# Performance work log

Hardware: AMD Instinct MI355X
Metric: run time of the kernel (lower is better)

The kernel has to match this reference:

```python
import jax, jax.numpy as jnp
import numpy as np


def _conv(x, kernel):
    # x: [N, C, H, W], kernel: [O, I, kh, kw]; torch conv2d padding=1 (symmetric both dims)
    return jax.lax.conv_general_dilated(
        x, kernel, window_strides=(1, 1), padding=((1, 1), (1, 1)),
        dimension_numbers=("NCHW", "OIHW", "NCHW"))


def setup_inputs() -> dict:
    key = jax.random.key(0)
    k1, k2 = jax.random.split(key)
    shape = (2, 7, 7, 3, 256, 256)  # bs, ah, aw, c, h, w
    infer = jax.random.normal(k1, shape, dtype=jnp.float32)
    ref = jax.random.normal(k2, shape, dtype=jnp.float32)
    return {"infer": infer, "ref": ref}


def reference(infer, ref):
    bs, ah, aw, c, h, w = infer.shape
    x = infer.reshape(bs * ah * aw, c, h, w)
    y = ref.reshape(bs * ah * aw, c, h, w)
    # fixed gradient kernels, identical across all 3x3 in/out channel pairs
    kh = jnp.broadcast_to(
        jnp.array([-0.5, 0.0, 0.5], jnp.float32).reshape(1, 1, 1, 3), (3, 3, 1, 3))
    kv = jnp.broadcast_to(
        jnp.array([-0.5, 0.0, 0.5], jnp.float32).reshape(1, 1, 3, 1), (3, 3, 3, 1))
    # torch padding=1 on a (1,3) kernel -> output (h+2, w); on (3,1) -> (h, w+2)
    loss_h = jnp.mean(jnp.abs(_conv(x, kh) - _conv(y, kh)))
    loss_v = jnp.mean(jnp.abs(_conv(x, kv) - _conv(y, kv)))
    return (loss_h + loss_v) / 2.0
```

## Files before the change

kernel.cpp:

```cpp
#include <hip/hip_runtime.h>


#define TH 32
#define NSTRIP 8
#define NIMG 98
#define W 256
#define IMG_CH_STRIDE 65536

__global__ __launch_bounds__(256) void detail_loss_kernel(
    const float* __restrict__ x, const float* __restrict__ y,
    float* __restrict__ out) {
  __shared__ float Dsh[TH + 2][W];

  const int n     = blockIdx.x / NSTRIP;
  const int strip = blockIdx.x % NSTRIP;
  const int h0    = strip * TH;
  const int tid   = threadIdx.x;
  const int sub   = tid >> 6;
  const int w4    = (tid & 63) << 2;

  const size_t img_off = (size_t)n * 3 * IMG_CH_STRIDE;
  const float* xb = x + img_off;
  const float* yb = y + img_off;

  for (int base = 0; base < TH + 2; base += 4) {
    int lr = base + sub;
    if (lr < TH + 2) {
      int row = h0 - 1 + lr;
      float4 d = make_float4(0.f, 0.f, 0.f, 0.f);
      if (row >= 0 && row < 256) {
        int off = row * W + w4;
        #pragma unroll
        for (int c = 0; c < 3; ++c) {
          float4 xv = *(const float4*)(xb + (size_t)c * IMG_CH_STRIDE + off);
          float4 yv = *(const float4*)(yb + (size_t)c * IMG_CH_STRIDE + off);
          d.x += xv.x - yv.x;
          d.y += xv.y - yv.y;
          d.z += xv.z - yv.z;
          d.w += xv.w - yv.w;
        }
      }
      *(float4*)&Dsh[lr][w4] = d;
    }
  }
  __syncthreads();

  const int w = tid;
  float acc = 0.f;
  #pragma unroll 4
  for (int r = 0; r < TH; ++r) {
    const float* rowp = Dsh[r + 1];
    float dl = (w >= 1)     ? rowp[w - 1] : 0.f;
    float dr = (w <= W - 2) ? rowp[w + 1] : 0.f;
    float du = Dsh[r][w];
    float dd = Dsh[r + 2][w];
    acc += fabsf(dr - dl) + fabsf(dd - du);
  }

  #pragma unroll
  for (int off = 32; off > 0; off >>= 1)
    acc += __shfl_down(acc, off, 64);

  __shared__ float wsum[4];
  if ((tid & 63) == 0) wsum[tid >> 6] = acc;
  __syncthreads();
  if (tid == 0) {
    float s = wsum[0] + wsum[1] + wsum[2] + wsum[3];
    atomicAdd(out, s * (0.25f / 6472704.0f));
  }
}

extern "C" void kernel_launch(void* const* d_in, const int* in_sizes, int n_in,
                              void* d_out, int out_size, void* d_ws, size_t ws_size,
                              hipStream_t stream) {
  const float* infer = (const float*)d_in[0];
  const float* ref   = (const float*)d_in[1];
  float* out = (float*)d_out;

  hipMemsetAsync(out, 0, sizeof(float), stream);
  detail_loss_kernel<<<NIMG * NSTRIP, 256, 0, stream>>>(infer, ref, out);
}
```

Measured before the change: 175.4 us.

## Compute one row per wavefront in registers with shuffles instead of shared-memory strips

Each wavefront now handles a single output row. It loads the three neighbouring rows for all channels directly into registers and gets horizontal neighbours with cross-lane shuffles, so the shared-memory strip tile and its barrier are gone. The grid grows from 784 to 6272 blocks. In exchange, each input row is re-read three times from global memory or cache, which raises traffic compared with the strip approach that reused halo rows, and there are eight times as many atomics.

```diff
diff --git a/kernel.cpp b/kernel.cpp
--- a/kernel.cpp
+++ b/kernel.cpp
@@ -1,68 +1,72 @@
 #include <hip/hip_runtime.h>
 
 
-#define TH 32
-#define NSTRIP 8
+#define W 256
 #define NIMG 98
-#define W 256
-#define IMG_CH_STRIDE 65536
+#define CH_STRIDE 65536
 
 __global__ __launch_bounds__(256) void detail_loss_kernel(
     const float* __restrict__ x, const float* __restrict__ y,
     float* __restrict__ out) {
-  __shared__ float Dsh[TH + 2][W];
+  const int tid  = threadIdx.x;
+  const int lane = tid & 63;
+  const int wv   = tid >> 6;
+  const int n    = blockIdx.x >> 6;
+  const int rg   = blockIdx.x & 63;
+  const int row  = rg * 4 + wv;
 
-  const int n     = blockIdx.x / NSTRIP;
-  const int strip = blockIdx.x % NSTRIP;
-  const int h0    = strip * TH;
-  const int tid   = threadIdx.x;
-  const int sub   = tid >> 6;
-  const int w4    = (tid & 63) << 2;
+  const float* xb = x + (size_t)n * 3 * CH_STRIDE + (lane << 2);
+  const float* yb = y + (size_t)n * 3 * CH_STRIDE + (lane << 2);
 
-  const size_t img_off = (size_t)n * 3 * IMG_CH_STRIDE;
-  const float* xb = x + img_off;
-  const float* yb = y + img_off;
-
-  for (int base = 0; base < TH + 2; base += 4) {
-    int lr = base + sub;
-    if (lr < TH + 2) {
-      int row = h0 - 1 + lr;
-      float4 d = make_float4(0.f, 0.f, 0.f, 0.f);
-      if (row >= 0 && row < 256) {
-        int off = row * W + w4;
-        #pragma unroll
-        for (int c = 0; c < 3; ++c) {
-          float4 xv = *(const float4*)(xb + (size_t)c * IMG_CH_STRIDE + off);
-          float4 yv = *(const float4*)(yb + (size_t)c * IMG_CH_STRIDE + off);
-          d.x += xv.x - yv.x;
-          d.y += xv.y - yv.y;
-          d.z += xv.z - yv.z;
-          d.w += xv.w - yv.w;
-        }
+  float4 xr[3][3], yr[3][3];
+  #pragma unroll
+  for (int dr = 0; dr < 3; ++dr) {
+    int r = row - 1 + dr;
+    bool ok = (r >= 0) && (r < 256);
+    #pragma unroll
+    for (int c = 0; c < 3; ++c) {
+      if (ok) {
+        int off = c * CH_STRIDE + r * W;
+        xr[dr][c] = *(const float4*)(xb + off);
+        yr[dr][c] = *(const float4*)(yb + off);
+      } else {
+        xr[dr][c] = make_float4(0.f, 0.f, 0.f, 0.f);
+        yr[dr][c] = make_float4(0.f, 0.f, 0.f, 0.f);
       }
-      *(float4*)&Dsh[lr][w4] = d;
     }
   }
-  __syncthreads();
 
-  const int w = tid;
-  float acc = 0.f;
-  #pragma unroll 4
-  for (int r = 0; r < TH; ++r) {
-    const float* rowp = Dsh[r + 1];
-    float dl = (w >= 1)     ? rowp[w - 1] : 0.f;
-    float dr = (w <= W - 2) ? rowp[w + 1] : 0.f;
-    float du = Dsh[r][w];
-    float dd = Dsh[r + 2][w];
-    acc += fabsf(dr - dl) + fabsf(dd - du);
+  float4 Dm, D0, Dp;
+  #pragma unroll
+  for (int dr = 0; dr < 3; ++dr) {
+    float4 d;
+    d.x = (xr[dr][0].x - yr[dr][0].x) + (xr[dr][1].x - yr[dr][1].x) + (xr[dr][2].x - yr[dr][2].x);
+    d.y = (xr[dr][0].y - yr[dr][0].y) + (xr[dr][1].y - yr[dr][1].y) + (xr[dr][2].y - yr[dr][2].y);
+    d.z = (xr[dr][0].z - yr[dr][0].z) + (xr[dr][1].z - yr[dr][1].z) + (xr[dr][2].z - yr[dr][2].z);
+    d.w = (xr[dr][0].w - yr[dr][0].w) + (xr[dr][1].w - yr[dr][1].w) + (xr[dr][2].w - yr[dr][2].w);
+    if (dr == 0) Dm = d; else if (dr == 1) D0 = d; else Dp = d;
   }
+
+  float left  = __shfl_up(D0.w, 1, 64);
+  float right = __shfl_down(D0.x, 1, 64);
+  if (lane == 0)  left  = 0.f;
+  if (lane == 63) right = 0.f;
+
+  float acc = fabsf(D0.y - left)
+            + fabsf(D0.z - D0.x)
+            + fabsf(D0.w - D0.y)
+            + fabsf(right - D0.z)
+            + fabsf(Dp.x - Dm.x)
+            + fabsf(Dp.y - Dm.y)
+            + fabsf(Dp.z - Dm.z)
+            + fabsf(Dp.w - Dm.w);
 
   #pragma unroll
   for (int off = 32; off > 0; off >>= 1)
     acc += __shfl_down(acc, off, 64);
 
   __shared__ float wsum[4];
-  if ((tid & 63) == 0) wsum[tid >> 6] = acc;
+  if (lane == 0) wsum[wv] = acc;
   __syncthreads();
   if (tid == 0) {
     float s = wsum[0] + wsum[1] + wsum[2] + wsum[3];
@@ -78,5 +82,5 @@
   float* out = (float*)d_out;
 
   hipMemsetAsync(out, 0, sizeof(float), stream);
-  detail_loss_kernel<<<NIMG * NSTRIP, 256, 0, stream>>>(infer, ref, out);
+  detail_loss_kernel<<<NIMG * 64, 256, 0, stream>>>(infer, ref, out);
 }
```

Measured after the change: 215.5 us. +22.8%, slower.

## Load halo rows with async global-to-LDS copies and two-stage reduction

Applied to the files above, without the earlier changes.

Each block now covers 8 rows instead of 32, and all six raw channel tiles (x and y, three channels each) are loaded straight into LDS with global_load_lds 16-byte copies rather than through registers. The channel-summed differences are held in registers for the vertical gradient and written to LDS only for the horizontal neighbours. The single atomic is replaced by per-block partial sums plus a second small reduction kernel when workspace is available. The aim is more memory-level parallelism and more blocks in flight. The cost is more halo re-reads (10 rows per 8 output rows), about 71 KB of LDS per block, which limits occupancy, and an extra kernel launch.

```diff
diff --git a/kernel.cpp b/kernel.cpp
--- a/kernel.cpp
+++ b/kernel.cpp
@@ -1,73 +1,115 @@
 #include <hip/hip_runtime.h>
 
 
-#define TH 32
-#define NSTRIP 8
+#define W 256
 #define NIMG 98
-#define W 256
-#define IMG_CH_STRIDE 65536
+#define CH_STRIDE 65536
+#define TH 8
+#define HALO (TH + 2)
+#define NSTRIP 32
+#define NBLK (NIMG * NSTRIP)
+#define SCALE (0.25f / 6472704.0f)
 
-__global__ __launch_bounds__(256) void detail_loss_kernel(
-    const float* __restrict__ x, const float* __restrict__ y,
-    float* __restrict__ out) {
-  __shared__ float Dsh[TH + 2][W];
+__device__ __forceinline__ void async_copy16(const float* g, float* l) {
+  __builtin_amdgcn_global_load_lds(
+      (const __attribute__((address_space(1))) void*)g,
+      (__attribute__((address_space(3))) void*)l,
+      16, 0, 0);
+}
 
-  const int n     = blockIdx.x / NSTRIP;
-  const int strip = blockIdx.x % NSTRIP;
-  const int h0    = strip * TH;
+struct SmemT {
+  float raw[6][HALO][W];
+  float Dsh[HALO][W];
+  float ws[4];
+};
+
+__device__ __forceinline__ float block_body(const float* __restrict__ x,
+                                            const float* __restrict__ y,
+                                            SmemT& sm) {
   const int tid   = threadIdx.x;
-  const int sub   = tid >> 6;
-  const int w4    = (tid & 63) << 2;
+  const int lane  = tid & 63;
+  const int wv    = tid >> 6;
+  const int b     = blockIdx.x;
+  const int n     = b >> 5;
+  const int strip = b & 31;
+  const int r0    = strip * TH;
 
-  const size_t img_off = (size_t)n * 3 * IMG_CH_STRIDE;
-  const float* xb = x + img_off;
-  const float* yb = y + img_off;
+  const float* xb = x + (size_t)n * 3 * CH_STRIDE;
+  const float* yb = y + (size_t)n * 3 * CH_STRIDE;
 
-  for (int base = 0; base < TH + 2; base += 4) {
-    int lr = base + sub;
-    if (lr < TH + 2) {
-      int row = h0 - 1 + lr;
-      float4 d = make_float4(0.f, 0.f, 0.f, 0.f);
-      if (row >= 0 && row < 256) {
-        int off = row * W + w4;
-        #pragma unroll
-        for (int c = 0; c < 3; ++c) {
-          float4 xv = *(const float4*)(xb + (size_t)c * IMG_CH_STRIDE + off);
-          float4 yv = *(const float4*)(yb + (size_t)c * IMG_CH_STRIDE + off);
-          d.x += xv.x - yv.x;
-          d.y += xv.y - yv.y;
-          d.z += xv.z - yv.z;
-          d.w += xv.w - yv.w;
-        }
-      }
-      *(float4*)&Dsh[lr][w4] = d;
-    }
+  #pragma unroll
+  for (int i = 0; i < 15; ++i) {
+    const int id = wv + 4 * i;
+    const int s  = id / HALO;
+    const int lr = id % HALO;
+    int g = r0 - 1 + lr;
+    g = (g < 0) ? 0 : (g > 255 ? 255 : g);
+    const float* gp = ((s < 3) ? (xb + s * CH_STRIDE) : (yb + (s - 3) * CH_STRIDE))
+                      + g * W + (lane << 2);
+    async_copy16(gp, &sm.raw[s][lr][0]);
   }
   __syncthreads();
 
   const int w = tid;
+  float d[HALO];
+  #pragma unroll
+  for (int lr = 0; lr < HALO; ++lr) {
+    const int g = r0 - 1 + lr;
+    float v = 0.f;
+    if (g >= 0 && g < 256) {
+      v = (sm.raw[0][lr][w] - sm.raw[3][lr][w])
+        + (sm.raw[1][lr][w] - sm.raw[4][lr][w])
+        + (sm.raw[2][lr][w] - sm.raw[5][lr][w]);
+    }
+    d[lr] = v;
+    sm.Dsh[lr][w] = v;
+  }
+  __syncthreads();
+
   float acc = 0.f;
-  #pragma unroll 4
+  #pragma unroll
   for (int r = 0; r < TH; ++r) {
-    const float* rowp = Dsh[r + 1];
-    float dl = (w >= 1)     ? rowp[w - 1] : 0.f;
-    float dr = (w <= W - 2) ? rowp[w + 1] : 0.f;
-    float du = Dsh[r][w];
-    float dd = Dsh[r + 2][w];
-    acc += fabsf(dr - dl) + fabsf(dd - du);
+    const float* rp = sm.Dsh[r + 1];
+    float left  = (w > 0)     ? rp[w - 1] : 0.f;
+    float right = (w < W - 1) ? rp[w + 1] : 0.f;
+    acc += fabsf(right - left) + fabsf(d[r + 2] - d[r]);
   }
 
   #pragma unroll
   for (int off = 32; off > 0; off >>= 1)
     acc += __shfl_down(acc, off, 64);
+  if (lane == 0) sm.ws[wv] = acc;
+  __syncthreads();
+  return sm.ws[0] + sm.ws[1] + sm.ws[2] + sm.ws[3];
+}
 
-  __shared__ float wsum[4];
-  if ((tid & 63) == 0) wsum[tid >> 6] = acc;
+__global__ __launch_bounds__(256) void detail_stage1(
+    const float* __restrict__ x, const float* __restrict__ y,
+    float* __restrict__ partial) {
+  __shared__ SmemT sm;
+  float s = block_body(x, y, sm);
+  if (threadIdx.x == 0) partial[blockIdx.x] = s;
+}
+
+__global__ __launch_bounds__(256) void detail_stage1_atomic(
+    const float* __restrict__ x, const float* __restrict__ y,
+    float* __restrict__ out) {
+  __shared__ SmemT sm;
+  float s = block_body(x, y, sm);
+  if (threadIdx.x == 0) atomicAdd(out, s * SCALE);
+}
+
+__global__ __launch_bounds__(256) void detail_stage2(
+    const float* __restrict__ partial, float* __restrict__ out) {
+  float acc = 0.f;
+  for (int i = threadIdx.x; i < NBLK; i += 256) acc += partial[i];
+  #pragma unroll
+  for (int off = 32; off > 0; off >>= 1)
+    acc += __shfl_down(acc, off, 64);
+  __shared__ float ws[4];
+  if ((threadIdx.x & 63) == 0) ws[threadIdx.x >> 6] = acc;
   __syncthreads();
-  if (tid == 0) {
-    float s = wsum[0] + wsum[1] + wsum[2] + wsum[3];
-    atomicAdd(out, s * (0.25f / 6472704.0f));
-  }
+  if (threadIdx.x == 0) out[0] = (ws[0] + ws[1] + ws[2] + ws[3]) * SCALE;
 }
 
 extern "C" void kernel_launch(void* const* d_in, const int* in_sizes, int n_in,
@@ -77,6 +119,12 @@
   const float* ref   = (const float*)d_in[1];
   float* out = (float*)d_out;
 
-  hipMemsetAsync(out, 0, sizeof(float), stream);
-  detail_loss_kernel<<<NIMG * NSTRIP, 256, 0, stream>>>(infer, ref, out);
+  if (ws_size >= NBLK * sizeof(float)) {
+    float* partial = (float*)d_ws;
+    detail_stage1<<<NBLK, 256, 0, stream>>>(infer, ref, partial);
+    detail_stage2<<<1, 256, 0, stream>>>(partial, out);
+  } else {
+    hipMemsetAsync(out, 0, sizeof(float), stream);
+    detail_stage1_atomic<<<NBLK, 256, 0, stream>>>(infer, ref, out);
+  }
 }
```

After: 167.3 us. 1.05x faster.
